# Optimization experiments

Measured on AMD Instinct MI355X. Metric: run time of the kernel, lower is better.

Reference implementation:

```python
import jax, jax.numpy as jnp
import numpy as np

K = 16  # kNN neighbors
R = 4   # upsampling ratio


def knn_idx(x, k):
    """Per-cloud kNN (self excluded). x: [B,N,C] -> idx [B,N,k] int32."""
    sq = jnp.sum(x * x, axis=-1)  # [B,N]
    d = sq[:, :, None] + sq[:, None, :] - 2.0 * jnp.einsum('bnc,bmc->bnm', x, x)
    n = x.shape[1]
    d = d + jnp.eye(n, dtype=x.dtype) * jnp.asarray(1e9, x.dtype)  # exclude self-loop
    _, idx = jax.lax.top_k(-d, k)  # k smallest distances
    return idx


def edge_conv(x, idx, W, b):
    """EdgeConv: mlp([x_i, x_j - x_i]) with max aggregation over neighbors.
    x: [B,N,C], idx: [B,N,k] -> [B,N,out]."""
    nbr = jax.vmap(lambda xb, ib: xb[ib])(x, idx)            # [B,N,k,C] gather
    ctr = jnp.broadcast_to(x[:, :, None, :], nbr.shape)
    e = jnp.concatenate([ctr, nbr - ctr], axis=-1)           # [B,N,k,2C]
    h = jax.nn.relu(jnp.einsum('bnkc,cd->bnkd', e, W) + b)
    return jnp.max(h, axis=2)                                # max aggregate


def setup_inputs() -> dict:
    key = jax.random.key(0)
    ks = jax.random.split(key, 16)
    B, N = 8, 2048
    chans = [3, 32, 32, 64]  # DynConv stack: 3->32->32->64
    C = chans[-1]

    def lin(k, fan_in, fan_out):
        s = 1.0 / np.sqrt(fan_in)
        return jax.random.uniform(k, (fan_in, fan_out), jnp.float32, -s, s)

    inp = {'x': jax.random.normal(ks[0], (B, N, 3), jnp.float32)}
    # DynConv (EdgeConv) weights: Linear(2*in, out)
    for i in range(3):
        inp[f'W{i}'] = lin(ks[1 + i], 2 * chans[i], chans[i + 1])
        inp[f'b{i}'] = jnp.zeros((chans[i + 1],), jnp.float32)
    # NodeShuffle: EdgeConv(C -> R*C) then shuffle N -> N*R
    inp['Wup'] = lin(ks[5], 2 * C, R * C)
    inp['bup'] = jnp.zeros((R * C,), jnp.float32)
    # Reconstructor MLP([64,128,64,3])
    rdims = [64, 128, 64, 3]
    for i in range(3):
        inp[f'Wr{i}'] = lin(ks[6 + i], rdims[i], rdims[i + 1])
        inp[f'br{i}'] = jnp.zeros((rdims[i + 1],), jnp.float32)
    return inp


def reference(x, W0, b0, W1, b1, W2, b2, Wup, bup, Wr0, br0, Wr1, br1, Wr2, br2):
    # Dynamic feature extractor: recompute kNN on current feature space each layer
    for W, b in ((W0, b0), (W1, b1), (W2, b2)):
        idx = knn_idx(x, K)
        x = edge_conv(x, idx, W, b)
    # NodeShuffle upsampler: EdgeConv to R*C channels, then shuffle nodes
    idx = knn_idx(x, K)
    h = edge_conv(x, idx, Wup, bup)              # [B,N,R*C]
    B, N, _ = h.shape
    C = h.shape[-1] // R
    x = h.reshape(B, N, R, C).reshape(B, N * R, C)  # [B,N*R,C]
    # Reconstructor MLP -> xyz
    x = jax.nn.relu(x @ Wr0 + br0)
    x = jax.nn.relu(x @ Wr1 + br1)
    return x @ Wr2 + br2                          # [B,N*R,3]
```

## Files before the change

kernel.cpp:

```cpp
#include <hip/hip_runtime.h>

#define B_ 8
#define N_ 2048
#define K_ 16
#define M_ (B_*N_)

__device__ __forceinline__ unsigned long long kmin(unsigned long long a, unsigned long long b) {
    return a < b ? a : b;
}

template<int C>
__global__ __launch_bounds__(256, 2) void knn_kernel(const float* __restrict__ X,
                                                     int* __restrict__ idx_out) {
    constexpr int ROWS = 32, TPR = 8, TJ = 128;
    constexpr int SJ = (C == 3) ? 4 : (C + 4);
    __shared__ float xj[TJ * SJ];

    int tid = threadIdx.x;
    int rlocal = tid / TPR;
    int r = tid & (TPR - 1);
    int m = blockIdx.x * ROWS + rlocal;
    int b = m >> 11;
    int i = m & (N_ - 1);

    const float* xrow = X + (size_t)m * C;
    float xi[C];
#pragma unroll
    for (int c = 0; c < C; ++c) xi[c] = xrow[c];

    unsigned long long t[16];
#pragma unroll
    for (int q = 0; q < 16; ++q) t[q] = ~0ull;

    const float* Xb = X + (size_t)b * N_ * C;

    for (int jt = 0; jt < N_ / TJ; ++jt) {
        __syncthreads();
        if constexpr (C == 3) {
            for (int e = tid; e < TJ * 3; e += 256)
                xj[(e / 3) * 4 + (e % 3)] = Xb[jt * TJ * 3 + e];
        } else {
            constexpr int C4 = C / 4;
            const float4* src = (const float4*)(Xb + (size_t)jt * TJ * C);
            for (int e4 = tid; e4 < TJ * C4; e4 += 256) {
                int jl = e4 / C4, c4 = e4 % C4;
                *(float4*)&xj[jl * SJ + c4 * 4] = src[e4];
            }
        }
        __syncthreads();

#pragma unroll 2
        for (int jl = r; jl < TJ; jl += TPR) {
            float s = 0.f;
            if constexpr (C == 3) {
#pragma unroll
                for (int c = 0; c < 3; ++c) {
                    float df = xi[c] - xj[jl * SJ + c];
                    s = fmaf(df, df, s);
                }
            } else {
#pragma unroll
                for (int c4 = 0; c4 < C / 4; ++c4) {
                    float4 v = *(const float4*)&xj[jl * SJ + c4 * 4];
                    float d0 = xi[c4 * 4 + 0] - v.x;
                    float d1 = xi[c4 * 4 + 1] - v.y;
                    float d2 = xi[c4 * 4 + 2] - v.z;
                    float d3 = xi[c4 * 4 + 3] - v.w;
                    s = fmaf(d0, d0, s);
                    s = fmaf(d1, d1, s);
                    s = fmaf(d2, d2, s);
                    s = fmaf(d3, d3, s);
                }
            }
            int jg = jt * TJ + jl;
            unsigned u = __float_as_uint(s);
            u ^= (unsigned)(((int)u >> 31) | 0x80000000);
            unsigned long long key = ((unsigned long long)u << 32) | (unsigned)jg;
            if (jg == i) key = ~0ull;
            if (key < t[15]) {
                t[15] = key;
#pragma unroll
                for (int s2 = 15; s2 > 0; --s2) {
                    unsigned long long a = t[s2 - 1], bb = t[s2];
                    bool sw = bb < a;
                    t[s2 - 1] = sw ? bb : a;
                    t[s2]     = sw ? a : bb;
                }
            }
        }
    }

#pragma unroll
    for (int msk = 1; msk <= 4; msk <<= 1) {
        unsigned long long o[16];
#pragma unroll
        for (int q = 0; q < 16; ++q)
            o[q] = __shfl_xor((unsigned long long)t[q], msk, 64);
        unsigned long long nt[16];
#pragma unroll
        for (int q = 0; q < 16; ++q) nt[q] = kmin(t[q], o[15 - q]);
#pragma unroll
        for (int s2 = 8; s2 >= 1; s2 >>= 1) {
#pragma unroll
            for (int q = 0; q < 16; ++q) {
                if (!(q & s2)) {
                    unsigned long long a = nt[q], bb = nt[q | s2];
                    bool sw = bb < a;
                    nt[q]      = sw ? bb : a;
                    nt[q | s2] = sw ? a : bb;
                }
            }
        }
#pragma unroll
        for (int q = 0; q < 16; ++q) t[q] = nt[q];
    }

    if (r == 0) {
        int* op = idx_out + (size_t)m * K_;
#pragma unroll
        for (int q = 0; q < 16; ++q) op[q] = (int)(unsigned)(t[q] & 0xffffffffull);
    }
}

template<int C, int D>
__global__ __launch_bounds__(256) void t1_kernel(const float* __restrict__ X,
                                                 const float* __restrict__ W,
                                                 double* __restrict__ T1) {
    constexpr int D4 = D / 4;
    int e4 = blockIdx.x * 256 + threadIdx.x;
    if (e4 >= M_ * D4) return;
    int m = e4 / D4, d4 = e4 - m * D4;
    const float* xr = X + (size_t)m * C;
    double a0 = 0.0, a1 = 0.0, a2 = 0.0, a3 = 0.0;
#pragma unroll
    for (int c = 0; c < C; ++c) {
        double a = (double)xr[c];
        float4 w = *(const float4*)&W[(size_t)c * D + d4 * 4];
        a0 = fma(a, (double)w.x, a0);
        a1 = fma(a, (double)w.y, a1);
        a2 = fma(a, (double)w.z, a2);
        a3 = fma(a, (double)w.w, a3);
    }
    double* op = &T1[(size_t)e4 * 4];
    op[0] = a0; op[1] = a1; op[2] = a2; op[3] = a3;
}

template<int C, int D, int TN>
__global__ __launch_bounds__(256) void gemm_max_kernel(
        const float* __restrict__ X, const double* __restrict__ T1,
        const float* __restrict__ W, const float* __restrict__ bias,
        const int* __restrict__ idx, float* __restrict__ O) {
    constexpr int CS  = (C == 3) ? 4 : C + 4;
    constexpr int LPR = TN / 4;
    constexpr int TW  = 256 / TN;
    constexpr int UR  = TN / 16;
    __shared__ float Xs[64 * CS];
    __shared__ float Ws[C * TN];
    __shared__ float Xi[4 * CS];
    __shared__ int   idxs[64];

    int tid = threadIdx.x;
    int m0p = blockIdx.x * 4;
    int n0  = blockIdx.y * TN;
    int b   = m0p >> 11;
    const float* Xb = X + ((size_t)b << 11) * C;
    const float* Wb = W + (size_t)C * D;

    if (tid < 64) idxs[tid] = idx[(size_t)m0p * K_ + tid];
    if (tid < 4 * C) {
        int pl = tid / C, c = tid - pl * C;
        Xi[pl * CS + c] = X[(size_t)(m0p + pl) * C + c];
    }
    __syncthreads();

    if constexpr (C == 3) {
        for (int e = tid; e < 64 * 3; e += 256) {
            int r = e / 3, c = e - r * 3;
            int j = idxs[r];
            Xs[r * CS + c] = Xb[(size_t)j * 3 + c] - Xi[(r >> 4) * CS + c];
        }
    } else {
        constexpr int C4 = C / 4;
        for (int e4 = tid; e4 < 64 * C4; e4 += 256) {
            int r = e4 / C4, c4 = e4 - r * C4;
            int j = idxs[r];
            float4 v  = *(const float4*)&Xb[(size_t)j * C + c4 * 4];
            float4 xc = *(const float4*)&Xi[(r >> 4) * CS + c4 * 4];
            v.x -= xc.x; v.y -= xc.y; v.z -= xc.z; v.w -= xc.w;
            *(float4*)&Xs[r * CS + c4 * 4] = v;
        }
    }
    for (int e = tid; e < C * TN; e += 256) {
        int cr = e / TN;
        Ws[e] = Wb[(size_t)cr * D + n0 + (e - cr * TN)];
    }
    __syncthreads();

    int tx = tid % LPR, ty = tid / LPR;
    int m = m0p + ty / TW;

    const double* t1p = &T1[(size_t)m * D + n0 + tx * 4];
    double t10 = t1p[0], t11 = t1p[1], t12 = t1p[2], t13 = t1p[3];
    double acc[UR][4];
#pragma unroll
    for (int u = 0; u < UR; ++u) {
        acc[u][0] = t10; acc[u][1] = t11; acc[u][2] = t12; acc[u][3] = t13;
    }

#pragma unroll 2
    for (int c = 0; c < C; ++c) {
        float4 w = *(const float4*)&Ws[c * TN + tx * 4];
        double w0 = (double)w.x, w1 = (double)w.y, w2 = (double)w.z, w3 = (double)w.w;
#pragma unroll
        for (int u = 0; u < UR; ++u) {
            double a = (double)Xs[(ty * UR + u) * CS + c];
            acc[u][0] = fma(a, w0, acc[u][0]);
            acc[u][1] = fma(a, w1, acc[u][1]);
            acc[u][2] = fma(a, w2, acc[u][2]);
            acc[u][3] = fma(a, w3, acc[u][3]);
        }
    }

    double bm[4];
#pragma unroll
    for (int q = 0; q < 4; ++q) bm[q] = acc[0][q];
#pragma unroll
    for (int u = 1; u < UR; ++u)
#pragma unroll
        for (int q = 0; q < 4; ++q) bm[q] = fmax(bm[q], acc[u][q]);

#pragma unroll
    for (int off = LPR; off < LPR * TW; off <<= 1)
#pragma unroll
        for (int q = 0; q < 4; ++q)
            bm[q] = fmax(bm[q], __shfl_xor(bm[q], off, 64));

    if (ty % TW == 0) {
        float4 bi = *(const float4*)&bias[n0 + tx * 4];
        float4 o;
        o.x = (float)fmax(bm[0] + (double)bi.x, 0.0);
        o.y = (float)fmax(bm[1] + (double)bi.y, 0.0);
        o.z = (float)fmax(bm[2] + (double)bi.z, 0.0);
        o.w = (float)fmax(bm[3] + (double)bi.w, 0.0);
        *(float4*)&O[(size_t)m * D + n0 + tx * 4] = o;
    }
}

__global__ __launch_bounds__(256) void recon_kernel(const float* __restrict__ U,
        const float* __restrict__ W0, const float* __restrict__ b0,
        const float* __restrict__ W1, const float* __restrict__ b1,
        const float* __restrict__ W2, const float* __restrict__ b2,
        float* __restrict__ O) {
    __shared__ float F[32 * 68];
    __shared__ float H1[128 * 33];
    __shared__ float H2[64 * 33];
    __shared__ float W2s[64 * 4];
    __shared__ float b0s[128], b1s[64], b2s[4];

    int tid = threadIdx.x;
    int m0 = blockIdx.x * 32;

    {
        const float4* src = (const float4*)(U + (size_t)m0 * 64);
        for (int e4 = tid; e4 < 32 * 16; e4 += 256) {
            int p = e4 >> 4, c4 = e4 & 15;
            *(float4*)&F[p * 68 + c4 * 4] = src[e4];
        }
    }
    if (tid < 192) W2s[(tid / 3) * 4 + (tid % 3)] = W2[tid];
    if (tid < 128) b0s[tid] = b0[tid];
    else if (tid < 192) b1s[tid - 128] = b1[tid - 128];
    else if (tid == 192) { b2s[0] = b2[0]; b2s[1] = b2[1]; b2s[2] = b2[2]; }
    __syncthreads();

    int p = tid >> 3, s = tid & 7;

    float acc[16];
#pragma unroll
    for (int q = 0; q < 16; ++q) acc[q] = 0.f;
    for (int c = 0; c < 64; ++c) {
        float a = F[p * 68 + c];
#pragma unroll
        for (int q = 0; q < 4; ++q) {
            float4 w = *(const float4*)&W0[c * 128 + s * 4 + q * 32];
            acc[q * 4 + 0] = fmaf(a, w.x, acc[q * 4 + 0]);
            acc[q * 4 + 1] = fmaf(a, w.y, acc[q * 4 + 1]);
            acc[q * 4 + 2] = fmaf(a, w.z, acc[q * 4 + 2]);
            acc[q * 4 + 3] = fmaf(a, w.w, acc[q * 4 + 3]);
        }
    }
#pragma unroll
    for (int q = 0; q < 4; ++q)
#pragma unroll
        for (int i2 = 0; i2 < 4; ++i2) {
            int dd = s * 4 + q * 32 + i2;
            H1[dd * 33 + p] = fmaxf(acc[q * 4 + i2] + b0s[dd], 0.f);
        }
    __syncthreads();

    float a2[8];
#pragma unroll
    for (int q = 0; q < 8; ++q) a2[q] = 0.f;
    for (int c = 0; c < 128; ++c) {
        float a = H1[c * 33 + p];
#pragma unroll
        for (int q = 0; q < 2; ++q) {
            float4 w = *(const float4*)&W1[c * 64 + s * 4 + q * 32];
            a2[q * 4 + 0] = fmaf(a, w.x, a2[q * 4 + 0]);
            a2[q * 4 + 1] = fmaf(a, w.y, a2[q * 4 + 1]);
            a2[q * 4 + 2] = fmaf(a, w.z, a2[q * 4 + 2]);
            a2[q * 4 + 3] = fmaf(a, w.w, a2[q * 4 + 3]);
        }
    }
#pragma unroll
    for (int q = 0; q < 2; ++q)
#pragma unroll
        for (int i2 = 0; i2 < 4; ++i2) {
            int dd = s * 4 + q * 32 + i2;
            H2[dd * 33 + p] = fmaxf(a2[q * 4 + i2] + b1s[dd], 0.f);
        }
    __syncthreads();

    if (tid < 96) {
        int p3 = tid / 3, d3 = tid - p3 * 3;
        float av = 0.f;
#pragma unroll
        for (int c = 0; c < 64; ++c)
            av = fmaf(H2[c * 33 + p3], W2s[c * 4 + d3], av);
        O[(size_t)(m0 + p3) * 3 + d3] = av + b2s[d3];
    }
}

extern "C" void kernel_launch(void* const* d_in, const int* in_sizes, int n_in,
                              void* d_out, int out_size, void* d_ws, size_t ws_size,
                              hipStream_t stream) {
    const float* x   = (const float*)d_in[0];
    const float* W0  = (const float*)d_in[1];
    const float* b0  = (const float*)d_in[2];
    const float* W1  = (const float*)d_in[3];
    const float* b1  = (const float*)d_in[4];
    const float* W2  = (const float*)d_in[5];
    const float* b2  = (const float*)d_in[6];
    const float* Wup = (const float*)d_in[7];
    const float* bup = (const float*)d_in[8];
    const float* Wr0 = (const float*)d_in[9];
    const float* br0 = (const float*)d_in[10];
    const float* Wr1 = (const float*)d_in[11];
    const float* br1 = (const float*)d_in[12];
    const float* Wr2 = (const float*)d_in[13];
    const float* br2 = (const float*)d_in[14];
    float* out = (float*)d_out;

    char* ws = (char*)d_ws;
    size_t o = 0;
    auto alloc = [&](size_t nbytes) {
        void* pp = ws + o;
        o += (nbytes + 255) & ~(size_t)255;
        return pp;
    };
    float*  X1  = (float*)alloc((size_t)M_ * 32 * 4);
    float*  X2  = (float*)alloc((size_t)M_ * 32 * 4);
    float*  X3  = (float*)alloc((size_t)M_ * 64 * 4);
    double* T1  = (double*)alloc((size_t)M_ * 256 * 8);
    float*  H   = (float*)alloc((size_t)M_ * 256 * 4);
    int*    idxb = (int*)alloc((size_t)M_ * 16 * 4);

    knn_kernel<3><<<512, 256, 0, stream>>>(x, idxb);
    t1_kernel<3, 32><<<M_ * 8 / 256, 256, 0, stream>>>(x, W0, T1);
    gemm_max_kernel<3, 32, 32><<<dim3(M_ / 4, 1), 256, 0, stream>>>(x, T1, W0, b0, idxb, X1);
    knn_kernel<32><<<512, 256, 0, stream>>>(X1, idxb);
    t1_kernel<32, 32><<<M_ * 8 / 256, 256, 0, stream>>>(X1, W1, T1);
    gemm_max_kernel<32, 32, 32><<<dim3(M_ / 4, 1), 256, 0, stream>>>(X1, T1, W1, b1, idxb, X2);
    knn_kernel<32><<<512, 256, 0, stream>>>(X2, idxb);
    t1_kernel<32, 64><<<M_ * 16 / 256, 256, 0, stream>>>(X2, W2, T1);
    gemm_max_kernel<32, 64, 64><<<dim3(M_ / 4, 1), 256, 0, stream>>>(X2, T1, W2, b2, idxb, X3);
    knn_kernel<64><<<512, 256, 0, stream>>>(X3, idxb);
    t1_kernel<64, 256><<<M_ * 64 / 256, 256, 0, stream>>>(X3, Wup, T1);
    gemm_max_kernel<64, 256, 64><<<dim3(M_ / 4, 4), 256, 0, stream>>>(X3, T1, Wup, bup, idxb, H);
    recon_kernel<<<2048, 256, 0, stream>>>(H, Wr0, br0, Wr1, br1, Wr2, br2, out);
}
```

Measured before the change: 1.299 ms.

## Tile kNN distances through shared memory and precompute per-point edge projections

```diff
diff --git a/kernel.cpp b/kernel.cpp
--- a/kernel.cpp
+++ b/kernel.cpp
@@ -5,245 +5,259 @@
 #define K_ 16
 #define M_ (B_*N_)
 
-__device__ __forceinline__ unsigned long long kmin(unsigned long long a, unsigned long long b) {
-    return a < b ? a : b;
-}
+typedef unsigned long long ull;
+
+__device__ __forceinline__ ull kmin(ull a, ull b) { return a < b ? a : b; }
 
 template<int C>
-__global__ __launch_bounds__(256, 2) void knn_kernel(const float* __restrict__ X,
-                                                     int* __restrict__ idx_out) {
-    constexpr int ROWS = 32, TPR = 8, TJ = 128;
-    constexpr int SJ = (C == 3) ? 4 : (C + 4);
-    __shared__ float xj[TJ * SJ];
+__global__ __launch_bounds__(256, 2) void knn2_kernel(const float* __restrict__ X,
+                                                      int* __restrict__ idx_out) {
+    constexpr int TJ = 128;
+    constexpr int SJ = TJ + 4;
+    constexpr int SS = TJ + 4;
+    constexpr int SI = 36;
+    __shared__ float xiT[C][SI];
+    __shared__ float xjT[C][SJ];
+    __shared__ float S[32][SS];
 
     int tid = threadIdx.x;
-    int rlocal = tid / TPR;
-    int r = tid & (TPR - 1);
-    int m = blockIdx.x * ROWS + rlocal;
-    int b = m >> 11;
-    int i = m & (N_ - 1);
-
-    const float* xrow = X + (size_t)m * C;
-    float xi[C];
-#pragma unroll
-    for (int c = 0; c < C; ++c) xi[c] = xrow[c];
-
-    unsigned long long t[16];
+    int sb = (blockIdx.x & 7) * (M_ / 32 / 8) + (blockIdx.x >> 3);
+    int m0 = sb * 32;
+    int b  = m0 >> 11;
+    int i0 = m0 & (N_ - 1);
+    const float* Xb = X + ((size_t)b << 11) * C;
+
+    if constexpr (C == 3) {
+        if (tid < 96) { int ir = tid / 3, c = tid - ir * 3;
+            xiT[c][ir] = X[(size_t)(m0 + ir) * 3 + c]; }
+    } else {
+        constexpr int C4 = C / 4;
+        for (int e4 = tid; e4 < 32 * C4; e4 += 256) {
+            int ir = e4 / C4, c4 = e4 - ir * C4;
+            float4 v = *(const float4*)&X[(size_t)(m0 + ir) * C + c4 * 4];
+            xiT[c4*4+0][ir] = v.x; xiT[c4*4+1][ir] = v.y;
+            xiT[c4*4+2][ir] = v.z; xiT[c4*4+3][ir] = v.w;
+        }
+    }
+
+    ull t[16];
 #pragma unroll
     for (int q = 0; q < 16; ++q) t[q] = ~0ull;
-
-    const float* Xb = X + (size_t)b * N_ * C;
+    float t15f = __uint_as_float(0x7FFFFFFFu);
+
+    int ig = tid >> 5, jl4 = tid & 31;
+    int irow = tid >> 3, r = tid & 7;
+    int i_loc = i0 + irow;
 
     for (int jt = 0; jt < N_ / TJ; ++jt) {
         __syncthreads();
         if constexpr (C == 3) {
-            for (int e = tid; e < TJ * 3; e += 256)
-                xj[(e / 3) * 4 + (e % 3)] = Xb[jt * TJ * 3 + e];
+            for (int e = tid; e < TJ * 3; e += 256) {
+                int jl = e / 3, c = e - jl * 3;
+                xjT[c][jl] = Xb[(size_t)jt * TJ * 3 + e];
+            }
         } else {
             constexpr int C4 = C / 4;
-            const float4* src = (const float4*)(Xb + (size_t)jt * TJ * C);
-            for (int e4 = tid; e4 < TJ * C4; e4 += 256) {
-                int jl = e4 / C4, c4 = e4 % C4;
-                *(float4*)&xj[jl * SJ + c4 * 4] = src[e4];
+            for (int e4 = tid; e4 < 32 * C4; e4 += 256) {
+                int jb = e4 / C4, c4 = e4 - jb * C4;
+                const float* src = &Xb[(size_t)(jt * TJ + jb * 4) * C + c4 * 4];
+                float4 v0 = *(const float4*)&src[0];
+                float4 v1 = *(const float4*)&src[C];
+                float4 v2 = *(const float4*)&src[2 * C];
+                float4 v3 = *(const float4*)&src[3 * C];
+                *(float4*)&xjT[c4*4+0][jb*4] = make_float4(v0.x, v1.x, v2.x, v3.x);
+                *(float4*)&xjT[c4*4+1][jb*4] = make_float4(v0.y, v1.y, v2.y, v3.y);
+                *(float4*)&xjT[c4*4+2][jb*4] = make_float4(v0.z, v1.z, v2.z, v3.z);
+                *(float4*)&xjT[c4*4+3][jb*4] = make_float4(v0.w, v1.w, v2.w, v3.w);
             }
         }
         __syncthreads();
 
-#pragma unroll 2
-        for (int jl = r; jl < TJ; jl += TPR) {
-            float s = 0.f;
-            if constexpr (C == 3) {
-#pragma unroll
-                for (int c = 0; c < 3; ++c) {
-                    float df = xi[c] - xj[jl * SJ + c];
-                    s = fmaf(df, df, s);
+        float acc[4][4];
+#pragma unroll
+        for (int u = 0; u < 4; ++u) {
+            acc[u][0] = 0.f; acc[u][1] = 0.f; acc[u][2] = 0.f; acc[u][3] = 0.f;
+        }
+#pragma unroll 4
+        for (int c = 0; c < C; ++c) {
+            float4 xi4 = *(const float4*)&xiT[c][ig * 4];
+            float4 xj4 = *(const float4*)&xjT[c][jl4 * 4];
+            float xiv[4] = {xi4.x, xi4.y, xi4.z, xi4.w};
+            float xjv[4] = {xj4.x, xj4.y, xj4.z, xj4.w};
+#pragma unroll
+            for (int u = 0; u < 4; ++u)
+#pragma unroll
+                for (int v = 0; v < 4; ++v) {
+                    float df = xiv[u] - xjv[v];
+                    acc[u][v] = fmaf(df, df, acc[u][v]);
                 }
-            } else {
-#pragma unroll
-                for (int c4 = 0; c4 < C / 4; ++c4) {
-                    float4 v = *(const float4*)&xj[jl * SJ + c4 * 4];
-                    float d0 = xi[c4 * 4 + 0] - v.x;
-                    float d1 = xi[c4 * 4 + 1] - v.y;
-                    float d2 = xi[c4 * 4 + 2] - v.z;
-                    float d3 = xi[c4 * 4 + 3] - v.w;
-                    s = fmaf(d0, d0, s);
-                    s = fmaf(d1, d1, s);
-                    s = fmaf(d2, d2, s);
-                    s = fmaf(d3, d3, s);
+        }
+#pragma unroll
+        for (int u = 0; u < 4; ++u)
+            *(float4*)&S[ig * 4 + u][jl4 * 4] =
+                make_float4(acc[u][0], acc[u][1], acc[u][2], acc[u][3]);
+        __syncthreads();
+
+        int jbase = jt * TJ + r * 16;
+#pragma unroll
+        for (int w = 0; w < 4; ++w) {
+            float4 sv = *(const float4*)&S[irow][r * 16 + w * 4];
+            float se[4] = {sv.x, sv.y, sv.z, sv.w};
+            float mn = fminf(fminf(se[0], se[1]), fminf(se[2], se[3]));
+            if (!(mn > t15f)) {
+#pragma unroll
+                for (int e = 0; e < 4; ++e) {
+                    float s = se[e];
+                    if (!(s > t15f)) {
+                        int jg = jbase + w * 4 + e;
+                        if (jg != i_loc) {
+                            unsigned uu = __float_as_uint(s) ^ 0x80000000u;
+                            ull key = ((ull)uu << 32) | (unsigned)jg;
+                            if (key < t[15]) {
+                                t[15] = key;
+#pragma unroll
+                                for (int s2 = 15; s2 > 0; --s2) {
+                                    ull a = t[s2 - 1], bb2 = t[s2];
+                                    bool sw = bb2 < a;
+                                    t[s2 - 1] = sw ? bb2 : a;
+                                    t[s2]     = sw ? a : bb2;
+                                }
+                                t15f = __uint_as_float((unsigned)(t[15] >> 32) ^ 0x80000000u);
+                            }
+                        }
+                    }
                 }
             }
-            int jg = jt * TJ + jl;
-            unsigned u = __float_as_uint(s);
-            u ^= (unsigned)(((int)u >> 31) | 0x80000000);
-            unsigned long long key = ((unsigned long long)u << 32) | (unsigned)jg;
-            if (jg == i) key = ~0ull;
-            if (key < t[15]) {
-                t[15] = key;
-#pragma unroll
-                for (int s2 = 15; s2 > 0; --s2) {
-                    unsigned long long a = t[s2 - 1], bb = t[s2];
-                    bool sw = bb < a;
-                    t[s2 - 1] = sw ? bb : a;
-                    t[s2]     = sw ? a : bb;
+        }
+    }
+
+#pragma unroll
+    for (int msk = 1; msk <= 4; msk <<= 1) {
+        ull o[16];
+#pragma unroll
+        for (int q = 0; q < 16; ++q)
+            o[q] = __shfl_xor((ull)t[q], msk, 64);
+        ull nt[16];
+#pragma unroll
+        for (int q = 0; q < 16; ++q) nt[q] = kmin(t[q], o[15 - q]);
+#pragma unroll
+        for (int s2 = 8; s2 >= 1; s2 >>= 1) {
+#pragma unroll
+            for (int q = 0; q < 16; ++q) {
+                if (!(q & s2)) {
+                    ull a = nt[q], bb2 = nt[q | s2];
+                    bool sw = bb2 < a;
+                    nt[q]      = sw ? bb2 : a;
+                    nt[q | s2] = sw ? a : bb2;
                 }
             }
         }
-    }
-
-#pragma unroll
-    for (int msk = 1; msk <= 4; msk <<= 1) {
-        unsigned long long o[16];
-#pragma unroll
-        for (int q = 0; q < 16; ++q)
-            o[q] = __shfl_xor((unsigned long long)t[q], msk, 64);
-        unsigned long long nt[16];
-#pragma unroll
-        for (int q = 0; q < 16; ++q) nt[q] = kmin(t[q], o[15 - q]);
-#pragma unroll
-        for (int s2 = 8; s2 >= 1; s2 >>= 1) {
-#pragma unroll
-            for (int q = 0; q < 16; ++q) {
-                if (!(q & s2)) {
-                    unsigned long long a = nt[q], bb = nt[q | s2];
-                    bool sw = bb < a;
-                    nt[q]      = sw ? bb : a;
-                    nt[q | s2] = sw ? a : bb;
-                }
-            }
-        }
 #pragma unroll
         for (int q = 0; q < 16; ++q) t[q] = nt[q];
     }
 
     if (r == 0) {
-        int* op = idx_out + (size_t)m * K_;
+        int* op = idx_out + (size_t)(m0 + irow) * K_;
 #pragma unroll
         for (int q = 0; q < 16; ++q) op[q] = (int)(unsigned)(t[q] & 0xffffffffull);
     }
 }
 
-template<int C, int D>
-__global__ __launch_bounds__(256) void t1_kernel(const float* __restrict__ X,
-                                                 const float* __restrict__ W,
-                                                 double* __restrict__ T1) {
-    constexpr int D4 = D / 4;
-    int e4 = blockIdx.x * 256 + threadIdx.x;
-    if (e4 >= M_ * D4) return;
-    int m = e4 / D4, d4 = e4 - m * D4;
-    const float* xr = X + (size_t)m * C;
-    double a0 = 0.0, a1 = 0.0, a2 = 0.0, a3 = 0.0;
-#pragma unroll
-    for (int c = 0; c < C; ++c) {
-        double a = (double)xr[c];
-        float4 w = *(const float4*)&W[(size_t)c * D + d4 * 4];
-        a0 = fma(a, (double)w.x, a0);
-        a1 = fma(a, (double)w.y, a1);
-        a2 = fma(a, (double)w.z, a2);
-        a3 = fma(a, (double)w.w, a3);
-    }
-    double* op = &T1[(size_t)e4 * 4];
-    op[0] = a0; op[1] = a1; op[2] = a2; op[3] = a3;
-}
-
-template<int C, int D, int TN>
-__global__ __launch_bounds__(256) void gemm_max_kernel(
-        const float* __restrict__ X, const double* __restrict__ T1,
-        const float* __restrict__ W, const float* __restrict__ bias,
-        const int* __restrict__ idx, float* __restrict__ O) {
-    constexpr int CS  = (C == 3) ? 4 : C + 4;
-    constexpr int LPR = TN / 4;
-    constexpr int TW  = 256 / TN;
-    constexpr int UR  = TN / 16;
-    __shared__ float Xs[64 * CS];
-    __shared__ float Ws[C * TN];
-    __shared__ float Xi[4 * CS];
-    __shared__ int   idxs[64];
-
+template<int C>
+__global__ __launch_bounds__(256) void proj_kernel(const float* __restrict__ X,
+        const float* __restrict__ W, double* __restrict__ T1NB,
+        int Dfull, int DH, int doff) {
+    __shared__ float XsT[C][68];
+    __shared__ float Bs[C][64];
     int tid = threadIdx.x;
-    int m0p = blockIdx.x * 4;
-    int n0  = blockIdx.y * TN;
-    int b   = m0p >> 11;
-    const float* Xb = X + ((size_t)b << 11) * C;
-    const float* Wb = W + (size_t)C * D;
-
-    if (tid < 64) idxs[tid] = idx[(size_t)m0p * K_ + tid];
-    if (tid < 4 * C) {
-        int pl = tid / C, c = tid - pl * C;
-        Xi[pl * CS + c] = X[(size_t)(m0p + pl) * C + c];
-    }
-    __syncthreads();
+    int m0 = blockIdx.x * 64;
+    int n0 = blockIdx.y * 64;
 
     if constexpr (C == 3) {
-        for (int e = tid; e < 64 * 3; e += 256) {
-            int r = e / 3, c = e - r * 3;
-            int j = idxs[r];
-            Xs[r * CS + c] = Xb[(size_t)j * 3 + c] - Xi[(r >> 4) * CS + c];
-        }
+        if (tid < 192) { int row = tid / 3, c = tid - row * 3;
+            XsT[c][row] = X[(size_t)(m0 + row) * 3 + c]; }
     } else {
         constexpr int C4 = C / 4;
         for (int e4 = tid; e4 < 64 * C4; e4 += 256) {
-            int r = e4 / C4, c4 = e4 - r * C4;
-            int j = idxs[r];
-            float4 v  = *(const float4*)&Xb[(size_t)j * C + c4 * 4];
-            float4 xc = *(const float4*)&Xi[(r >> 4) * CS + c4 * 4];
-            v.x -= xc.x; v.y -= xc.y; v.z -= xc.z; v.w -= xc.w;
-            *(float4*)&Xs[r * CS + c4 * 4] = v;
-        }
-    }
-    for (int e = tid; e < C * TN; e += 256) {
-        int cr = e / TN;
-        Ws[e] = Wb[(size_t)cr * D + n0 + (e - cr * TN)];
-    }
-    __syncthreads();
-
-    int tx = tid % LPR, ty = tid / LPR;
-    int m = m0p + ty / TW;
-
-    const double* t1p = &T1[(size_t)m * D + n0 + tx * 4];
-    double t10 = t1p[0], t11 = t1p[1], t12 = t1p[2], t13 = t1p[3];
-    double acc[UR][4];
-#pragma unroll
-    for (int u = 0; u < UR; ++u) {
-        acc[u][0] = t10; acc[u][1] = t11; acc[u][2] = t12; acc[u][3] = t13;
-    }
-
-#pragma unroll 2
+            int row = e4 / C4, c4 = e4 - row * C4;
+            float4 v = *(const float4*)&X[(size_t)(m0 + row) * C + c4 * 4];
+            XsT[c4*4+0][row] = v.x; XsT[c4*4+1][row] = v.y;
+            XsT[c4*4+2][row] = v.z; XsT[c4*4+3][row] = v.w;
+        }
+    }
+    for (int e = tid; e < C * 64; e += 256) {
+        int c = e >> 6, dc = e & 63;
+        int n = n0 + dc;
+        float wv = (n < DH) ? W[(size_t)c * Dfull + doff + n]
+                            : W[(size_t)(C + c) * Dfull + doff + (n - DH)];
+        Bs[c][dc] = wv;
+    }
+    __syncthreads();
+
+    int tx = tid & 15, ty = tid >> 4;
+    double acc[4][4];
+#pragma unroll
+    for (int u = 0; u < 4; ++u) { acc[u][0]=0.0; acc[u][1]=0.0; acc[u][2]=0.0; acc[u][3]=0.0; }
+
+#pragma unroll 4
     for (int c = 0; c < C; ++c) {
-        float4 w = *(const float4*)&Ws[c * TN + tx * 4];
-        double w0 = (double)w.x, w1 = (double)w.y, w2 = (double)w.z, w3 = (double)w.w;
-#pragma unroll
-        for (int u = 0; u < UR; ++u) {
-            double a = (double)Xs[(ty * UR + u) * CS + c];
-            acc[u][0] = fma(a, w0, acc[u][0]);
-            acc[u][1] = fma(a, w1, acc[u][1]);
-            acc[u][2] = fma(a, w2, acc[u][2]);
-            acc[u][3] = fma(a, w3, acc[u][3]);
-        }
-    }
-
-    double bm[4];
-#pragma unroll
-    for (int q = 0; q < 4; ++q) bm[q] = acc[0][q];
-#pragma unroll
-    for (int u = 1; u < UR; ++u)
-#pragma unroll
-        for (int q = 0; q < 4; ++q) bm[q] = fmax(bm[q], acc[u][q]);
-
-#pragma unroll
-    for (int off = LPR; off < LPR * TW; off <<= 1)
-#pragma unroll
-        for (int q = 0; q < 4; ++q)
-            bm[q] = fmax(bm[q], __shfl_xor(bm[q], off, 64));
-
-    if (ty % TW == 0) {
-        float4 bi = *(const float4*)&bias[n0 + tx * 4];
-        float4 o;
-        o.x = (float)fmax(bm[0] + (double)bi.x, 0.0);
-        o.y = (float)fmax(bm[1] + (double)bi.y, 0.0);
-        o.z = (float)fmax(bm[2] + (double)bi.z, 0.0);
-        o.w = (float)fmax(bm[3] + (double)bi.w, 0.0);
-        *(float4*)&O[(size_t)m * D + n0 + tx * 4] = o;
-    }
+        float4 xv = *(const float4*)&XsT[c][ty * 4];
+        float4 wv = *(const float4*)&Bs[c][tx * 4];
+        double xd[4] = {(double)xv.x, (double)xv.y, (double)xv.z, (double)xv.w};
+        double wd[4] = {(double)wv.x, (double)wv.y, (double)wv.z, (double)wv.w};
+#pragma unroll
+        for (int u = 0; u < 4; ++u)
+#pragma unroll
+            for (int v = 0; v < 4; ++v)
+                acc[u][v] = fma(xd[u], wd[v], acc[u][v]);
+    }
+#pragma unroll
+    for (int u = 0; u < 4; ++u) {
+        double* dst = &T1NB[(size_t)(m0 + ty * 4 + u) * (2 * DH) + n0 + tx * 4];
+        *(double2*)&dst[0] = make_double2(acc[u][0], acc[u][1]);
+        *(double2*)&dst[2] = make_double2(acc[u][2], acc[u][3]);
+    }
+}
+
+template<int DH>
+__global__ __launch_bounds__(256) void gmax_kernel(const double* __restrict__ T1NB,
+        const int* __restrict__ idx, const float* __restrict__ bias,
+        float* __restrict__ O, int Dfull, int doff) {
+    constexpr int TPP = DH / 2;
+    constexpr int PPB = 256 / TPP;
+    __shared__ int idxs[PPB * 16];
+
+    int tid = threadIdx.x;
+    int cpx = gridDim.x >> 3;
+    int sb = ((int)blockIdx.x & 7) * cpx + ((int)blockIdx.x >> 3);
+    int m0 = sb * PPB;
+
+    if (tid < PPB * 16)
+        idxs[tid] = idx[(size_t)(m0 + tid / 16) * K_ + (tid & 15)];
+    __syncthreads();
+
+    int p = tid / TPP, dh = tid % TPP;
+    int d0 = dh * 2;
+    int m = m0 + p;
+    int b = m >> 11;
+    size_t base = (size_t)m * (2 * DH);
+    double2 t1  = *(const double2*)&T1NB[base + d0];
+    double2 nbi = *(const double2*)&T1NB[base + DH + d0];
+    double ba = t1.x - nbi.x, bb = t1.y - nbi.y;
+    double ma = -1.0e300, mb = -1.0e300;
+    size_t rowb = ((size_t)(b << 11)) * (2 * DH) + DH + d0;
+    const int* ip = &idxs[p * 16];
+#pragma unroll 4
+    for (int k = 0; k < 16; ++k) {
+        int j = ip[k];
+        double2 q = *(const double2*)&T1NB[rowb + (size_t)j * (2 * DH)];
+        ma = fmax(ma, ba + q.x);
+        mb = fmax(mb, bb + q.y);
+    }
+    float2 o;
+    o.x = (float)fmax(ma + (double)bias[doff + d0],     0.0);
+    o.y = (float)fmax(mb + (double)bias[doff + d0 + 1], 0.0);
+    *(float2*)&O[(size_t)m * Dfull + doff + d0] = o;
 }
 
 __global__ __launch_bounds__(256) void recon_kernel(const float* __restrict__ U,
@@ -358,24 +372,26 @@
         o += (nbytes + 255) & ~(size_t)255;
         return pp;
     };
-    float*  X1  = (float*)alloc((size_t)M_ * 32 * 4);
-    float*  X2  = (float*)alloc((size_t)M_ * 32 * 4);
-    float*  X3  = (float*)alloc((size_t)M_ * 64 * 4);
-    double* T1  = (double*)alloc((size_t)M_ * 256 * 8);
-    float*  H   = (float*)alloc((size_t)M_ * 256 * 4);
+    float*  X1   = (float*)alloc((size_t)M_ * 32 * 4);
+    float*  X2   = (float*)alloc((size_t)M_ * 32 * 4);
+    float*  X3   = (float*)alloc((size_t)M_ * 64 * 4);
+    float*  H    = (float*)alloc((size_t)M_ * 256 * 4);
     int*    idxb = (int*)alloc((size_t)M_ * 16 * 4);
-
-    knn_kernel<3><<<512, 256, 0, stream>>>(x, idxb);
-    t1_kernel<3, 32><<<M_ * 8 / 256, 256, 0, stream>>>(x, W0, T1);
-    gemm_max_kernel<3, 32, 32><<<dim3(M_ / 4, 1), 256, 0, stream>>>(x, T1, W0, b0, idxb, X1);
-    knn_kernel<32><<<512, 256, 0, stream>>>(X1, idxb);
-    t1_kernel<32, 32><<<M_ * 8 / 256, 256, 0, stream>>>(X1, W1, T1);
-    gemm_max_kernel<32, 32, 32><<<dim3(M_ / 4, 1), 256, 0, stream>>>(X1, T1, W1, b1, idxb, X2);
-    knn_kernel<32><<<512, 256, 0, stream>>>(X2, idxb);
-    t1_kernel<32, 64><<<M_ * 16 / 256, 256, 0, stream>>>(X2, W2, T1);
-    gemm_max_kernel<32, 64, 64><<<dim3(M_ / 4, 1), 256, 0, stream>>>(X2, T1, W2, b2, idxb, X3);
-    knn_kernel<64><<<512, 256, 0, stream>>>(X3, idxb);
-    t1_kernel<64, 256><<<M_ * 64 / 256, 256, 0, stream>>>(X3, Wup, T1);
-    gemm_max_kernel<64, 256, 64><<<dim3(M_ / 4, 4), 256, 0, stream>>>(X3, T1, Wup, bup, idxb, H);
+    double* T1NB = (double*)alloc((size_t)M_ * 256 * 8);
+
+    knn2_kernel<3><<<512, 256, 0, stream>>>(x, idxb);
+    proj_kernel<3><<<dim3(M_ / 64, 1), 256, 0, stream>>>(x, W0, T1NB, 32, 32, 0);
+    gmax_kernel<32><<<M_ / 16, 256, 0, stream>>>(T1NB, idxb, b0, X1, 32, 0);
+    knn2_kernel<32><<<512, 256, 0, stream>>>(X1, idxb);
+    proj_kernel<32><<<dim3(M_ / 64, 1), 256, 0, stream>>>(X1, W1, T1NB, 32, 32, 0);
+    gmax_kernel<32><<<M_ / 16, 256, 0, stream>>>(T1NB, idxb, b1, X2, 32, 0);
+    knn2_kernel<32><<<512, 256, 0, stream>>>(X2, idxb);
+    proj_kernel<32><<<dim3(M_ / 64, 2), 256, 0, stream>>>(X2, W2, T1NB, 64, 64, 0);
+    gmax_kernel<64><<<M_ / 8, 256, 0, stream>>>(T1NB, idxb, b2, X3, 64, 0);
+    knn2_kernel<64><<<512, 256, 0, stream>>>(X3, idxb);
+    proj_kernel<64><<<dim3(M_ / 64, 4), 256, 0, stream>>>(X3, Wup, T1NB, 256, 128, 0);
+    gmax_kernel<128><<<M_ / 4, 256, 0, stream>>>(T1NB, idxb, bup, H, 256, 0);
+    proj_kernel<64><<<dim3(M_ / 64, 4), 256, 0, stream>>>(X3, Wup, T1NB, 256, 128, 128);
+    gmax_kernel<128><<<M_ / 4, 256, 0, stream>>>(T1NB, idxb, bup, H, 256, 128);
     recon_kernel<<<2048, 256, 0, stream>>>(H, Wr0, br0, Wr1, br1, Wr2, br2, out);
 }
```

Result: faster. 1.115 ms (-14.1%).
